# Optimization experiments

Hardware: AMD Instinct MI355X
Metric: run time of the kernel (lower is better)

Reference implementation:

```python
import jax, jax.numpy as jnp
from jax import lax
import numpy as np

B, N, F_IN = 8, 8192, 64
NPOINT, K = 2048, 16
C0 = F_IN + 3  # use_xyz concat
EPS = 1e-5


def setup_inputs() -> dict:
    key = jax.random.key(0)
    ks = jax.random.split(key, 8)
    xyz = jax.random.normal(ks[0], (B, 3, N), dtype=jnp.float32)
    points = jax.random.normal(ks[1], (B, F_IN, N), dtype=jnp.float32)
    def conv_params(k, cout, cin):
        W = jax.random.normal(k, (cout, cin), dtype=jnp.float32) * (1.0 / np.sqrt(cin))
        return W, jnp.zeros((cout,), jnp.float32)
    W1, b1 = conv_params(ks[2], 64, C0)
    W2, b2 = conv_params(ks[3], 64, 64)
    W3, b3 = conv_params(ks[4], 128, 64)
    g1 = jnp.ones((64,), jnp.float32); be1 = jnp.zeros((64,), jnp.float32)
    g2 = jnp.ones((64,), jnp.float32); be2 = jnp.zeros((64,), jnp.float32)
    return dict(xyz=xyz, points=points, W1=W1, b1=b1, g1=g1, be1=be1,
                W2=W2, b2=b2, g2=g2, be2=be2, W3=W3, b3=b3)


def _fps(xyz_bn3, npoint):
    # furthest point sampling; starts at index 0 (as PointNet++ CUDA op)
    b, n, _ = xyz_bn3.shape
    init_idx = jnp.zeros((b,), jnp.int32)
    dist0 = jnp.full((b, n), 1e10, xyz_bn3.dtype)

    def body(carry, _):
        dist, last = carry
        p = jnp.take_along_axis(xyz_bn3, last[:, None, None], axis=1)  # (b,1,3)
        d = jnp.sum((xyz_bn3 - p) ** 2, axis=-1)                       # (b,n)
        dist = jnp.minimum(dist, d)
        nxt = jnp.argmax(dist, axis=-1).astype(jnp.int32)
        return (dist, nxt), nxt

    (_, _), rest = lax.scan(body, (dist0, init_idx), None, length=npoint - 1)
    return jnp.concatenate([init_idx[None], rest], axis=0).T  # (b, npoint)


def _gather_feat(feat, idx):
    # feat: (B,C,N), idx: (B,...) -> (B,C,...)
    return jax.vmap(lambda f, i: f[:, i])(feat, idx)


def _conv_bn_relu(x, W, b, g, be):
    # 1x1 Conv2d + BatchNorm2d(training batch stats) + ReLU
    y = jnp.einsum('oi,bipk->bopk', W, x) + b[None, :, None, None]
    mean = y.mean(axis=(0, 2, 3))
    var = y.var(axis=(0, 2, 3))
    y = (y - mean[None, :, None, None]) * lax.rsqrt(var + EPS)[None, :, None, None]
    y = y * g[None, :, None, None] + be[None, :, None, None]
    return jax.nn.relu(y)


def reference(xyz, points, W1, b1, g1, be1, W2, b2, g2, be2, W3, b3):
    # --- sample_and_group_knn ---
    xyz_t = jnp.transpose(xyz, (0, 2, 1))             # (B,N,3)
    fps_idx = _fps(xyz_t, NPOINT)                      # (B,npoint)
    new_xyz = _gather_feat(xyz, fps_idx)               # (B,3,npoint)
    q = jnp.transpose(new_xyz, (0, 2, 1))              # (B,npoint,3)
    # squared distances (B,npoint,N)
    sq = (jnp.sum(q ** 2, -1)[:, :, None]
          + jnp.sum(xyz_t ** 2, -1)[:, None, :]
          - 2.0 * jnp.einsum('bqc,bnc->bqn', q, xyz_t))
    _, idx = lax.top_k(-sq, K)                         # (B,npoint,K) nearest
    grouped_xyz = _gather_feat(xyz, idx)               # (B,3,npoint,K)
    grouped_xyz = grouped_xyz - new_xyz[:, :, :, None]
    grouped_pts = _gather_feat(points, idx)            # (B,f,npoint,K)
    new_points = jnp.concatenate([grouped_xyz, grouped_pts], axis=1)  # (B,67,npoint,K)
    # --- shared MLP (1x1 convs) + max-pool over neighbors ---
    h = _conv_bn_relu(new_points, W1, b1, g1, be1)
    h = _conv_bn_relu(h, W2, b2, g2, be2)
    h = jnp.einsum('oi,bipk->bopk', W3, h) + b3[None, :, None, None]  # no bn/act
    new_feat = jnp.max(h, axis=3)                      # (B,128,npoint)
    return new_xyz, new_feat
```

## Files before the change

### kernel.cpp

```cpp
#include <hip/hip_runtime.h>
#pragma clang fp contract(off)

#define BB 8
#define NN 8192
#define NP 2048
#define KNbr 16
#define FIN 64
#define NPOS (BB*NP*KNbr)

typedef float f32x2 __attribute__((ext_vector_type(2)));
typedef unsigned long long u64;

__device__ __forceinline__ float sq3(float x, float y, float z) {
  return __fadd_rn(__fadd_rn(__fmul_rn(x,x), __fmul_rn(y,y)), __fmul_rn(z,z));
}

__device__ __forceinline__ int wave_imax(int x) {
  x = max(x, __builtin_amdgcn_update_dpp(0, x, 0x111, 0xf, 0xf, false));
  x = max(x, __builtin_amdgcn_update_dpp(0, x, 0x112, 0xf, 0xf, false));
  x = max(x, __builtin_amdgcn_update_dpp(0, x, 0x114, 0xf, 0xf, false));
  x = max(x, __builtin_amdgcn_update_dpp(0, x, 0x118, 0xf, 0xf, false));
  x = max(x, __builtin_amdgcn_update_dpp(0, x, 0x142, 0xa, 0xf, false));
  x = max(x, __builtin_amdgcn_update_dpp(0, x, 0x143, 0xc, 0xf, false));
  return __builtin_amdgcn_readlane(x, 63);
}
__device__ __forceinline__ unsigned wave_umin(unsigned x) {
  x = min(x, (unsigned)__builtin_amdgcn_update_dpp(-1, (int)x, 0x111, 0xf, 0xf, false));
  x = min(x, (unsigned)__builtin_amdgcn_update_dpp(-1, (int)x, 0x112, 0xf, 0xf, false));
  x = min(x, (unsigned)__builtin_amdgcn_update_dpp(-1, (int)x, 0x114, 0xf, 0xf, false));
  x = min(x, (unsigned)__builtin_amdgcn_update_dpp(-1, (int)x, 0x118, 0xf, 0xf, false));
  x = min(x, (unsigned)__builtin_amdgcn_update_dpp(-1, (int)x, 0x142, 0xa, 0xf, false));
  x = min(x, (unsigned)__builtin_amdgcn_update_dpp(-1, (int)x, 0x143, 0xc, 0xf, false));
  return (unsigned)__builtin_amdgcn_readlane((int)x, 63);
}

__global__ __launch_bounds__(256,1) void k_front(const float* __restrict__ xyz,
                                                 const float* __restrict__ pts,
                                                 const float* __restrict__ W1,
                                                 const float* __restrict__ b1,
                                                 float4* __restrict__ xyzw,
                                                 float4* __restrict__ qw,
                                                 float* __restrict__ pre,
                                                 float* __restrict__ stats,
                                                 float* __restrict__ newxyz) {
  __shared__ float tx[NN], ty[NN], tz[NN];
  __shared__ float4 res[NP];
  __shared__ u64 skey[2][4];
  int blk = blockIdx.x, tid = threadIdx.x;

  if (blk >= 8) {
    int g = (blk-8)*256 + tid;
    int b = g >> 13, n = g & (NN-1);
    const float* p = xyz + (size_t)b*3*NN;
    float x = p[n], y = p[NN+n], z = p[2*NN+n];
    xyzw[g] = make_float4(x, y, z, sq3(x,y,z));
    if (blk == 8) stats[tid] = 0.f;
    const float* P = pts + (size_t)b*FIN*NN + n;
    float pv[64];
    #pragma unroll
    for (int i=0;i<64;++i) pv[i] = P[(size_t)i*NN];
    float4* outp = (float4*)(pre + (size_t)g*64);
    for (int og=0; og<16; ++og) {
      float acc[4];
      #pragma unroll
      for (int oo=0;oo<4;++oo) {
        int o = og*4+oo;
        float s = b1[o];
        #pragma unroll
        for (int i=0;i<64;++i) s = fmaf(W1[o*67+3+i], pv[i], s);
        acc[oo] = s;
      }
      outp[og] = make_float4(acc[0],acc[1],acc[2],acc[3]);
    }
    return;
  }

  int b = blk;
  const float* pxyz = xyz + (size_t)b*3*NN;
  f32x2 px[16], py[16], pz[16], d2[16];
  #pragma unroll
  for (int j=0;j<16;++j) {
    int i = j*512 + 2*tid;
    float2 xv = *(const float2*)(pxyz + i);
    float2 yv = *(const float2*)(pxyz + NN + i);
    float2 zv = *(const float2*)(pxyz + 2*NN + i);
    tx[i] = xv.x; tx[i+1] = xv.y;
    ty[i] = yv.x; ty[i+1] = yv.y;
    tz[i] = zv.x; tz[i+1] = zv.y;
    px[j] = f32x2{xv.x, xv.y};
    py[j] = f32x2{yv.x, yv.y};
    pz[j] = f32x2{zv.x, zv.y};
    d2[j] = f32x2{1e10f, 1e10f};
  }
  float cx = pxyz[0], cy = pxyz[NN], cz = pxyz[2*NN];
  if (tid==0) res[0] = make_float4(cx, cy, cz, __int_as_float(0));
  int w = tid>>6;
  __syncthreads();
  for (int t=1;t<NP;++t) {
    f32x2 cx2 = {cx,cx}, cy2 = {cy,cy}, cz2 = {cz,cz};
    #pragma unroll
    for (int j=0;j<16;++j) {
      f32x2 dx = px[j]-cx2, dy = py[j]-cy2, dz = pz[j]-cz2;
      f32x2 dd = (dx*dx + dy*dy) + dz*dz;
#if __has_builtin(__builtin_elementwise_min)
      d2[j] = __builtin_elementwise_min(d2[j], dd);
#else
      d2[j].x = fminf(d2[j].x, dd.x);
      d2[j].y = fminf(d2[j].y, dd.y);
#endif
    }
    float tv[16]; int tk[16];
    #pragma unroll
    for (int j=0;j<16;++j) {
      bool r = d2[j].y > d2[j].x;
      tv[j] = r ? d2[j].y : d2[j].x;
      tk[j] = r ? 2*j+1 : 2*j;
    }
    #pragma unroll
    for (int j=0;j<8;++j) { bool r = tv[j+8] > tv[j]; if (r){tv[j]=tv[j+8]; tk[j]=tk[j+8];} }
    #pragma unroll
    for (int j=0;j<4;++j) { bool r = tv[j+4] > tv[j]; if (r){tv[j]=tv[j+4]; tk[j]=tk[j+4];} }
    #pragma unroll
    for (int j=0;j<2;++j) { bool r = tv[j+2] > tv[j]; if (r){tv[j]=tv[j+2]; tk[j]=tk[j+2];} }
    bool rr = tv[1] > tv[0];
    float lmax = rr ? tv[1] : tv[0];
    int   k    = rr ? tk[1] : tk[0];
    unsigned gidx = (unsigned)((k>>1)*512 + 2*tid + (k&1));
    int mb = wave_imax(__float_as_int(lmax));
    unsigned cand = (__float_as_int(lmax) == mb) ? gidx : 0xFFFFFFFFu;
    unsigned wwin = wave_umin(cand);
    int buf = t & 1;
    if ((tid & 63) == 0)
      skey[buf][w] = ((u64)(unsigned)mb << 32) | (u64)(0xFFFFFFFFu - wwin);
    __syncthreads();
    u64 mk = skey[buf][0];
    if (skey[buf][1] > mk) mk = skey[buf][1];
    if (skey[buf][2] > mk) mk = skey[buf][2];
    if (skey[buf][3] > mk) mk = skey[buf][3];
    unsigned widx = 0xFFFFFFFFu - (unsigned)(mk & 0xFFFFFFFFull);
    cx = tx[widx]; cy = ty[widx]; cz = tz[widx];
    if (tid == (t & 255))
      res[t] = make_float4(cx, cy, cz, __int_as_float((int)widx));
  }
  __syncthreads();
  float* outx = newxyz + (size_t)b*3*NP;
  #pragma unroll
  for (int s=0;s<8;++s) {
    int i = s*256 + tid;
    float4 r = res[i];
    qw[b*NP + i] = make_float4(r.x, r.y, r.z, sq3(r.x, r.y, r.z));
    outx[i] = r.x; outx[NP + i] = r.y; outx[2*NP + i] = r.z;
  }
}

__global__ __launch_bounds__(256) void k_knn(const float4* __restrict__ xyzw,
                                             const float4* __restrict__ qw,
                                             int* __restrict__ knnid) {
  int wave = threadIdx.x >> 6, lane = threadIdx.x & 63;
  int q = blockIdx.x*4 + wave;
  int b = q >> 11;
  float4 Q = qw[q];
  const float4* base = xyzw + (size_t)b*NN;
  float ld = 3.0e38f; int li = 0x7fffffff;
  float taud = 3.0e38f; int taui = 0x7fffffff;
  for (int c = 0; c < 128; ++c) {
    int idx = c*64 + lane;
    float4 P = base[idx];
    float dot = __fadd_rn(__fadd_rn(__fmul_rn(P.x,Q.x), __fmul_rn(P.y,Q.y)), __fmul_rn(P.z,Q.z));
    float dd  = __fsub_rn(__fadd_rn(Q.w, P.w), __fmul_rn(2.0f, dot));
    bool better = (dd < taud) || (dd == taud && idx < taui);
    u64 mask = __ballot(better);
    while (mask) {
      int src = __ffsll(mask) - 1;
      mask &= mask - 1;
      float bd = __shfl(dd, src, 64);
      int   bi = __shfl(idx, src, 64);
      bool before = (ld < bd) || (ld == bd && li < bi);
      float sd = __shfl_up(ld, 1, 64);
      int   si = __shfl_up(li, 1, 64);
      int   bp = __shfl_up((int)before, 1, 64);
      bool take_new = !before && (lane == 0 || bp);
      float nd = before ? ld : (take_new ? bd : sd);
      int   ni = before ? li : (take_new ? bi : si);
      if (lane < 16) { ld = nd; li = ni; }
      taud = __shfl(ld, 15, 64);
      taui = __shfl(li, 15, 64);
    }
  }
  if (lane < 16) knnid[q*16 + lane] = li;
}

__global__ __launch_bounds__(256) void k_y1(const float4* __restrict__ xyzw,
                                            const float4* __restrict__ qw,
                                            const int* __restrict__ knn,
                                            const float* __restrict__ pre,
                                            const float* __restrict__ W1,
                                            float* __restrict__ y) {
  int pos = blockIdx.x*256 + threadIdx.x;
  int bq = pos >> 4;
  int b  = pos >> 15;
  int n  = knn[pos];
  float4 Q = qw[bq];
  float4 P = xyzw[(b<<13) + n];
  float dx = __fsub_rn(P.x,Q.x), dy = __fsub_rn(P.y,Q.y), dz = __fsub_rn(P.z,Q.z);
  const float4* pr = (const float4*)(pre + ((size_t)(b<<13)+n)*64);
  float4* out = (float4*)(y + (size_t)pos*64);
  for (int og=0; og<16; ++og) {
    float4 acc = pr[og];
    float a[4] = {acc.x, acc.y, acc.z, acc.w};
    #pragma unroll
    for (int oo=0;oo<4;++oo) {
      int o = og*4+oo;
      a[oo] = fmaf(W1[o*67+0], dx, fmaf(W1[o*67+1], dy, fmaf(W1[o*67+2], dz, a[oo])));
    }
    out[og] = make_float4(a[0],a[1],a[2],a[3]);
  }
}

__global__ __launch_bounds__(256) void k_stats(const float* __restrict__ y,
                                               float* __restrict__ st) {
  __shared__ float s1[256], s2[256];
  int tid = threadIdx.x; int c = tid & 63, r = tid >> 6;
  size_t base = (size_t)blockIdx.x * 1024;
  float sum = 0.f, ss = 0.f;
  for (int i=0;i<256;++i) {
    float v = y[(base + (size_t)i*4 + r)*64 + c];
    sum += v; ss = fmaf(v, v, ss);
  }
  s1[tid]=sum; s2[tid]=ss;
  __syncthreads();
  if (tid < 64) {
    float t1 = s1[tid]+s1[tid+64]+s1[tid+128]+s1[tid+192];
    float t2 = s2[tid]+s2[tid+64]+s2[tid+128]+s2[tid+192];
    atomicAdd(&st[tid], t1);
    atomicAdd(&st[64+tid], t2);
  }
}

__global__ __launch_bounds__(256) void k_act(float* __restrict__ y,
                                             const float* __restrict__ st,
                                             const float* __restrict__ gam,
                                             const float* __restrict__ bet) {
  __shared__ __align__(16) float sS[64], sT[64];
  int tid = threadIdx.x;
  if (tid < 64) {
    float mean = st[tid] * (1.0f/NPOS);
    float var  = st[64+tid] * (1.0f/NPOS) - mean*mean;
    float istd = 1.0f / sqrtf(var + 1e-5f);
    float s = gam[tid]*istd;
    sS[tid] = s;
    sT[tid] = bet[tid] - mean*s;
  }
  __syncthreads();
  size_t g = (size_t)blockIdx.x*256 + tid;
  float4* Y = (float4*)y;
  #pragma unroll
  for (int r=0;r<4;++r) {
    size_t f4 = g + (size_t)r*1048576;
    int c0 = (int)((f4*4) & 63);
    float4 s4 = *(const float4*)(sS + c0);
    float4 t4 = *(const float4*)(sT + c0);
    float4 v = Y[f4];
    v.x = fmaxf(0.f, fmaf(v.x, s4.x, t4.x));
    v.y = fmaxf(0.f, fmaf(v.y, s4.y, t4.y));
    v.z = fmaxf(0.f, fmaf(v.z, s4.z, t4.z));
    v.w = fmaxf(0.f, fmaf(v.w, s4.w, t4.w));
    Y[f4] = v;
  }
}

__device__ __forceinline__ float dot64(const float4* x, const float* W, float init) {
  float a0 = init, a1 = 0.f, a2 = 0.f, a3 = 0.f;
  #pragma unroll
  for (int j=0;j<16;++j) {
    float4 v = x[j];
    a0 = fmaf(v.x, W[4*j],   a0);
    a1 = fmaf(v.y, W[4*j+1], a1);
    a2 = fmaf(v.z, W[4*j+2], a2);
    a3 = fmaf(v.w, W[4*j+3], a3);
  }
  return (a0+a1)+(a2+a3);
}

__global__ __launch_bounds__(256) void k_conv2v(float* __restrict__ y,
                                                const float* __restrict__ W2,
                                                const float* __restrict__ b2,
                                                float* __restrict__ st2) {
  __shared__ float r1[4][64], r2[4][64];
  int wave = threadIdx.x>>6;
  int wid = blockIdx.x*4 + wave;
  int lane = threadIdx.x & 63;
  float W[64];
  #pragma unroll
  for (int j=0;j<16;++j) {
    float4 t = *(const float4*)(W2 + (size_t)lane*64 + j*4);
    W[4*j]=t.x; W[4*j+1]=t.y; W[4*j+2]=t.z; W[4*j+3]=t.w;
  }
  float bb = b2[lane];
  size_t p0 = (size_t)wid*128;
  const float4* src = (const float4*)(y + p0*64);
  float4 xa[16], xb[16];
  float sum = 0.f, ss = 0.f;
  #pragma unroll
  for (int j=0;j<16;++j) xa[j] = src[j];
  for (int p=0;p<128;p+=2) {
    #pragma unroll
    for (int j=0;j<16;++j) xb[j] = src[(p+1)*16 + j];
    float acc = dot64(xa, W, bb);
    y[(p0+p)*64 + lane] = acc;
    sum += acc; ss = fmaf(acc, acc, ss);
    if (p+2 < 128) {
      #pragma unroll
      for (int j=0;j<16;++j) xa[j] = src[(p+2)*16 + j];
    }
    float acc2 = dot64(xb, W, bb);
    y[(p0+p+1)*64 + lane] = acc2;
    sum += acc2; ss = fmaf(acc2, acc2, ss);
  }
  r1[wave][lane] = sum; r2[wave][lane] = ss;
  __syncthreads();
  if (threadIdx.x < 64) {
    int l = threadIdx.x;
    float t1 = r1[0][l]+r1[1][l]+r1[2][l]+r1[3][l];
    float t2 = r2[0][l]+r2[1][l]+r2[2][l]+r2[3][l];
    atomicAdd(&st2[l], t1);
    atomicAdd(&st2[64+l], t2);
  }
}

__global__ __launch_bounds__(256) void k_c3v(const float* __restrict__ y,
                                             const float* __restrict__ W3,
                                             const float* __restrict__ b3,
                                             float* __restrict__ feat) {
  int wid = blockIdx.x*4 + (threadIdx.x>>6);
  int lane = threadIdx.x & 63;
  int h = wid & 1, chunk = wid >> 1;
  float W[64];
  #pragma unroll
  for (int j=0;j<16;++j) {
    float4 t = *(const float4*)(W3 + ((size_t)(h*64+lane))*64 + j*4);
    W[4*j]=t.x; W[4*j+1]=t.y; W[4*j+2]=t.z; W[4*j+3]=t.w;
  }
  float bb = b3[h*64+lane];
  const float4* src = (const float4*)(y + (size_t)chunk*16*16*64);
  float4 xa[16], xb[16];
  #pragma unroll
  for (int j=0;j<16;++j) xa[j] = src[j];
  int pos = 0;
  for (int q=0;q<16;++q) {
    float m = -3.0e38f;
    #pragma unroll 1
    for (int k=0;k<16;k+=2) {
      #pragma unroll
      for (int j=0;j<16;++j) xb[j] = src[(pos+1)*16 + j];
      m = fmaxf(m, dot64(xa, W, bb));
      if (pos+2 < 256) {
        #pragma unroll
        for (int j=0;j<16;++j) xa[j] = src[(pos+2)*16 + j];
      }
      m = fmaxf(m, dot64(xb, W, bb));
      pos += 2;
    }
    int gq = chunk*16 + q;
    int b = gq >> 11, qq = gq & (NP-1);
    feat[((size_t)(b*128 + h*64 + lane))*NP + qq] = m;
  }
}

extern "C" void kernel_launch(void* const* d_in, const int* in_sizes, int n_in,
                              void* d_out, int out_size, void* d_ws, size_t ws_size,
                              hipStream_t stream) {
  const float* xyz = (const float*)d_in[0];
  const float* pts = (const float*)d_in[1];
  const float* W1  = (const float*)d_in[2];
  const float* b1  = (const float*)d_in[3];
  const float* g1  = (const float*)d_in[4];
  const float* be1 = (const float*)d_in[5];
  const float* W2  = (const float*)d_in[6];
  const float* b2  = (const float*)d_in[7];
  const float* g2  = (const float*)d_in[8];
  const float* be2 = (const float*)d_in[9];
  const float* W3  = (const float*)d_in[10];
  const float* b3  = (const float*)d_in[11];
  float* out = (float*)d_out;
  float* ws  = (float*)d_ws;

  float4* xyzw  = (float4*)ws;
  float4* qw    = (float4*)(ws + 262144);
  int*    knnid = (int*)(ws + 344064);
  float*  pre   = ws + 1654784;
  float*  ybuf  = ws + 5849088;
  float*  stats = ws + 22626304;

  k_front <<<264, 256, 0, stream>>>(xyz, pts, W1, b1, xyzw, qw, pre, stats, out);
  k_knn   <<<4096, 256, 0, stream>>>(xyzw, qw, knnid);
  k_y1    <<<1024, 256, 0, stream>>>(xyzw, qw, knnid, pre, W1, ybuf);
  k_stats <<<256, 256, 0, stream>>>(ybuf, stats);
  k_act   <<<4096, 256, 0, stream>>>(ybuf, stats, g1, be1);
  k_conv2v<<<512, 256, 0, stream>>>(ybuf, W2, b2, stats + 128);
  k_act   <<<4096, 256, 0, stream>>>(ybuf, stats + 128, g2, be2);
  k_c3v   <<<512, 256, 0, stream>>>(ybuf, W3, b3, out + 49152);
}
```

Measured before the change: 2.621 ms.

## Overlap KNN grouping with FPS via persistent consumer blocks and progress flags

Merges the FPS front kernel, KNN search, first-layer grouping and BN statistics into one persistent launch. Eight blocks run FPS and publish query points plus a per-batch progress counter. The other 248 blocks first compute the pointwise W1 projection, then wait on a grid-wide flag barrier. They then poll the progress counters and run KNN, the xyz-offset conv and the stat accumulation for each query as soon as it is published. This hides the serial FPS latency behind the KNN work and removes several kernel launches and the knn-index and stats passes. The risks are that correctness depends on all blocks being co-resident, and that the progress and barrier flags are never reset between calls, so on repeated calls consumers may proceed on stale state.

Result: no change. 2.594 ms (-1.0%).

```diff
diff --git a/kernel.cpp b/kernel.cpp
--- a/kernel.cpp
+++ b/kernel.cpp
@@ -7,6 +7,8 @@
 #define KNbr 16
 #define FIN 64
 #define NPOS (BB*NP*KNbr)
+#define NCONS 248
+#define AG __HIP_MEMORY_SCOPE_AGENT
 
 typedef float f32x2 __attribute__((ext_vector_type(2)));
 typedef unsigned long long u64;
@@ -34,44 +36,123 @@
   return (unsigned)__builtin_amdgcn_readlane((int)x, 63);
 }
 
-__global__ __launch_bounds__(256,1) void k_front(const float* __restrict__ xyz,
-                                                 const float* __restrict__ pts,
-                                                 const float* __restrict__ W1,
-                                                 const float* __restrict__ b1,
-                                                 float4* __restrict__ xyzw,
-                                                 float4* __restrict__ qw,
-                                                 float* __restrict__ pre,
-                                                 float* __restrict__ stats,
-                                                 float* __restrict__ newxyz) {
+__device__ __forceinline__ void qstore4(float* p, float x, float y, float z, float w) {
+  __hip_atomic_store(p+0, x, __ATOMIC_RELAXED, AG);
+  __hip_atomic_store(p+1, y, __ATOMIC_RELAXED, AG);
+  __hip_atomic_store(p+2, z, __ATOMIC_RELAXED, AG);
+  __hip_atomic_store(p+3, w, __ATOMIC_RELAXED, AG);
+}
+
+__global__ __launch_bounds__(256,1) void k_front2(const float* __restrict__ xyz,
+                                                  const float* __restrict__ pts,
+                                                  const float* __restrict__ W1,
+                                                  const float* __restrict__ b1,
+                                                  float4* __restrict__ xyzw,
+                                                  float* __restrict__ qwf,
+                                                  float* __restrict__ pre,
+                                                  float* __restrict__ stats,
+                                                  int* __restrict__ prog,
+                                                  int* __restrict__ pflag,
+                                                  float* __restrict__ ybuf,
+                                                  float* __restrict__ newxyz) {
   __shared__ float tx[NN], ty[NN], tz[NN];
   __shared__ float4 res[NP];
   __shared__ u64 skey[2][4];
   int blk = blockIdx.x, tid = threadIdx.x;
+  int lane = tid & 63, wave = tid >> 6;
 
   if (blk >= 8) {
-    int g = (blk-8)*256 + tid;
-    int b = g >> 13, n = g & (NN-1);
-    const float* p = xyz + (size_t)b*3*NN;
-    float x = p[n], y = p[NN+n], z = p[2*NN+n];
-    xyzw[g] = make_float4(x, y, z, sq3(x,y,z));
+    for (int g = (blk-8)*256 + tid; g < BB*NN; g += NCONS*256) {
+      int b = g >> 13, n = g & (NN-1);
+      const float* p = xyz + (size_t)b*3*NN;
+      float x = p[n], y = p[NN+n], z = p[2*NN+n];
+      xyzw[g] = make_float4(x, y, z, sq3(x,y,z));
+      const float* P = pts + (size_t)b*FIN*NN + n;
+      float pv[64];
+      #pragma unroll
+      for (int i=0;i<64;++i) pv[i] = P[(size_t)i*NN];
+      float4* outp = (float4*)(pre + (size_t)g*64);
+      for (int og=0; og<16; ++og) {
+        float acc[4];
+        #pragma unroll
+        for (int oo=0;oo<4;++oo) {
+          int o = og*4+oo;
+          float s = b1[o];
+          #pragma unroll
+          for (int i=0;i<64;++i) s = fmaf(W1[o*67+3+i], pv[i], s);
+          acc[oo] = s;
+        }
+        outp[og] = make_float4(acc[0],acc[1],acc[2],acc[3]);
+      }
+    }
     if (blk == 8) stats[tid] = 0.f;
-    const float* P = pts + (size_t)b*FIN*NN + n;
-    float pv[64];
-    #pragma unroll
-    for (int i=0;i<64;++i) pv[i] = P[(size_t)i*NN];
-    float4* outp = (float4*)(pre + (size_t)g*64);
-    for (int og=0; og<16; ++og) {
-      float acc[4];
-      #pragma unroll
-      for (int oo=0;oo<4;++oo) {
-        int o = og*4+oo;
-        float s = b1[o];
-        #pragma unroll
-        for (int i=0;i<64;++i) s = fmaf(W1[o*67+3+i], pv[i], s);
-        acc[oo] = s;
+    __syncthreads();
+    if (tid == 0) {
+      __threadfence();
+      __hip_atomic_store(&pflag[blk-8], 1, __ATOMIC_RELEASE, AG);
+    }
+    bool ok = false;
+    while (!ok) {
+      int v = 1;
+      for (int i = lane; i < NCONS; i += 64)
+        v &= (__hip_atomic_load(&pflag[i], __ATOMIC_RELAXED, AG) == 1);
+      ok = (bool)__all(v);
+      if (!ok) __builtin_amdgcn_s_sleep(32);
+    }
+    __threadfence();
+
+    int slot = (blk-8)*4 + wave;
+    float W1a = W1[lane*67+0], W1b = W1[lane*67+1], W1c = W1[lane*67+2];
+    float sum = 0.f, ss = 0.f;
+    for (int qi = slot; qi < BB*NP; qi += NCONS*4) {
+      int t = qi >> 3, b = qi & 7;
+      while (__hip_atomic_load(&prog[b], __ATOMIC_RELAXED, AG) <= t)
+        __builtin_amdgcn_s_sleep(16);
+      const float* qp = qwf + ((size_t)(b*NP + t))*4;
+      float qx  = __hip_atomic_load(qp+0, __ATOMIC_RELAXED, AG);
+      float qy  = __hip_atomic_load(qp+1, __ATOMIC_RELAXED, AG);
+      float qz  = __hip_atomic_load(qp+2, __ATOMIC_RELAXED, AG);
+      float qw4 = __hip_atomic_load(qp+3, __ATOMIC_RELAXED, AG);
+      const float4* base = xyzw + (size_t)b*NN;
+      float ld = 3.0e38f; int li = 0x7fffffff;
+      float taud = 3.0e38f; int taui = 0x7fffffff;
+      for (int c = 0; c < 128; ++c) {
+        int idx = c*64 + lane;
+        float4 P = base[idx];
+        float dot = __fadd_rn(__fadd_rn(__fmul_rn(P.x,qx), __fmul_rn(P.y,qy)), __fmul_rn(P.z,qz));
+        float dd  = __fsub_rn(__fadd_rn(qw4, P.w), __fmul_rn(2.0f, dot));
+        bool better = (dd < taud) || (dd == taud && idx < taui);
+        u64 mask = __ballot(better);
+        while (mask) {
+          int src = __ffsll(mask) - 1;
+          mask &= mask - 1;
+          float bd = __shfl(dd, src, 64);
+          int   bi = __shfl(idx, src, 64);
+          bool before = (ld < bd) || (ld == bd && li < bi);
+          float sd = __shfl_up(ld, 1, 64);
+          int   si = __shfl_up(li, 1, 64);
+          int   bp = __shfl_up((int)before, 1, 64);
+          bool take_new = !before && (lane == 0 || bp);
+          float nd = before ? ld : (take_new ? bd : sd);
+          int   ni = before ? li : (take_new ? bi : si);
+          if (lane < 16) { ld = nd; li = ni; }
+          taud = __shfl(ld, 15, 64);
+          taui = __shfl(li, 15, 64);
+        }
       }
-      outp[og] = make_float4(acc[0],acc[1],acc[2],acc[3]);
-    }
+      const float* preb = pre + (size_t)b*NN*64;
+      float* yb = ybuf + ((size_t)(b*NP + t))*16*64;
+      for (int l=0;l<16;++l) {
+        int n = __shfl(li, l, 64);
+        float4 P = base[n];
+        float dx=__fsub_rn(P.x,qx), dy=__fsub_rn(P.y,qy), dz=__fsub_rn(P.z,qz);
+        float v = fmaf(W1a, dx, fmaf(W1b, dy, fmaf(W1c, dz, preb[(size_t)n*64 + lane])));
+        yb[l*64 + lane] = v;
+        sum += v; ss = fmaf(v, v, ss);
+      }
+    }
+    atomicAdd(&stats[lane], sum);
+    atomicAdd(&stats[64+lane], ss);
     return;
   }
 
@@ -93,7 +174,11 @@
     d2[j] = f32x2{1e10f, 1e10f};
   }
   float cx = pxyz[0], cy = pxyz[NN], cz = pxyz[2*NN];
-  if (tid==0) res[0] = make_float4(cx, cy, cz, __int_as_float(0));
+  if (tid==0) {
+    res[0] = make_float4(cx, cy, cz, 0.f);
+    qstore4(qwf + (size_t)(b*NP)*4, cx, cy, cz, sq3(cx,cy,cz));
+    __hip_atomic_store(&prog[b], 1, __ATOMIC_RELEASE, AG);
+  }
   int w = tid>>6;
   __syncthreads();
   for (int t=1;t<NP;++t) {
@@ -133,107 +218,27 @@
     if ((tid & 63) == 0)
       skey[buf][w] = ((u64)(unsigned)mb << 32) | (u64)(0xFFFFFFFFu - wwin);
     __syncthreads();
+    if ((t & 7) == 0 && tid == 0)
+      __hip_atomic_store(&prog[b], t, __ATOMIC_RELEASE, AG);
     u64 mk = skey[buf][0];
     if (skey[buf][1] > mk) mk = skey[buf][1];
     if (skey[buf][2] > mk) mk = skey[buf][2];
     if (skey[buf][3] > mk) mk = skey[buf][3];
     unsigned widx = 0xFFFFFFFFu - (unsigned)(mk & 0xFFFFFFFFull);
     cx = tx[widx]; cy = ty[widx]; cz = tz[widx];
-    if (tid == (t & 255))
-      res[t] = make_float4(cx, cy, cz, __int_as_float((int)widx));
+    if (tid == (t & 255)) {
+      res[t] = make_float4(cx, cy, cz, 0.f);
+      qstore4(qwf + ((size_t)(b*NP + t))*4, cx, cy, cz, sq3(cx,cy,cz));
+    }
   }
   __syncthreads();
+  if (tid == 0) __hip_atomic_store(&prog[b], NP, __ATOMIC_RELEASE, AG);
   float* outx = newxyz + (size_t)b*3*NP;
   #pragma unroll
   for (int s=0;s<8;++s) {
     int i = s*256 + tid;
     float4 r = res[i];
-    qw[b*NP + i] = make_float4(r.x, r.y, r.z, sq3(r.x, r.y, r.z));
     outx[i] = r.x; outx[NP + i] = r.y; outx[2*NP + i] = r.z;
-  }
-}
-
-__global__ __launch_bounds__(256) void k_knn(const float4* __restrict__ xyzw,
-                                             const float4* __restrict__ qw,
-                                             int* __restrict__ knnid) {
-  int wave = threadIdx.x >> 6, lane = threadIdx.x & 63;
-  int q = blockIdx.x*4 + wave;
-  int b = q >> 11;
-  float4 Q = qw[q];
-  const float4* base = xyzw + (size_t)b*NN;
-  float ld = 3.0e38f; int li = 0x7fffffff;
-  float taud = 3.0e38f; int taui = 0x7fffffff;
-  for (int c = 0; c < 128; ++c) {
-    int idx = c*64 + lane;
-    float4 P = base[idx];
-    float dot = __fadd_rn(__fadd_rn(__fmul_rn(P.x,Q.x), __fmul_rn(P.y,Q.y)), __fmul_rn(P.z,Q.z));
-    float dd  = __fsub_rn(__fadd_rn(Q.w, P.w), __fmul_rn(2.0f, dot));
-    bool better = (dd < taud) || (dd == taud && idx < taui);
-    u64 mask = __ballot(better);
-    while (mask) {
-      int src = __ffsll(mask) - 1;
-      mask &= mask - 1;
-      float bd = __shfl(dd, src, 64);
-      int   bi = __shfl(idx, src, 64);
-      bool before = (ld < bd) || (ld == bd && li < bi);
-      float sd = __shfl_up(ld, 1, 64);
-      int   si = __shfl_up(li, 1, 64);
-      int   bp = __shfl_up((int)before, 1, 64);
-      bool take_new = !before && (lane == 0 || bp);
-      float nd = before ? ld : (take_new ? bd : sd);
-      int   ni = before ? li : (take_new ? bi : si);
-      if (lane < 16) { ld = nd; li = ni; }
-      taud = __shfl(ld, 15, 64);
-      taui = __shfl(li, 15, 64);
-    }
-  }
-  if (lane < 16) knnid[q*16 + lane] = li;
-}
-
-__global__ __launch_bounds__(256) void k_y1(const float4* __restrict__ xyzw,
-                                            const float4* __restrict__ qw,
-                                            const int* __restrict__ knn,
-                                            const float* __restrict__ pre,
-                                            const float* __restrict__ W1,
-                                            float* __restrict__ y) {
-  int pos = blockIdx.x*256 + threadIdx.x;
-  int bq = pos >> 4;
-  int b  = pos >> 15;
-  int n  = knn[pos];
-  float4 Q = qw[bq];
-  float4 P = xyzw[(b<<13) + n];
-  float dx = __fsub_rn(P.x,Q.x), dy = __fsub_rn(P.y,Q.y), dz = __fsub_rn(P.z,Q.z);
-  const float4* pr = (const float4*)(pre + ((size_t)(b<<13)+n)*64);
-  float4* out = (float4*)(y + (size_t)pos*64);
-  for (int og=0; og<16; ++og) {
-    float4 acc = pr[og];
-    float a[4] = {acc.x, acc.y, acc.z, acc.w};
-    #pragma unroll
-    for (int oo=0;oo<4;++oo) {
-      int o = og*4+oo;
-      a[oo] = fmaf(W1[o*67+0], dx, fmaf(W1[o*67+1], dy, fmaf(W1[o*67+2], dz, a[oo])));
-    }
-    out[og] = make_float4(a[0],a[1],a[2],a[3]);
-  }
-}
-
-__global__ __launch_bounds__(256) void k_stats(const float* __restrict__ y,
-                                               float* __restrict__ st) {
-  __shared__ float s1[256], s2[256];
-  int tid = threadIdx.x; int c = tid & 63, r = tid >> 6;
-  size_t base = (size_t)blockIdx.x * 1024;
-  float sum = 0.f, ss = 0.f;
-  for (int i=0;i<256;++i) {
-    float v = y[(base + (size_t)i*4 + r)*64 + c];
-    sum += v; ss = fmaf(v, v, ss);
-  }
-  s1[tid]=sum; s2[tid]=ss;
-  __syncthreads();
-  if (tid < 64) {
-    float t1 = s1[tid]+s1[tid+64]+s1[tid+128]+s1[tid+192];
-    float t2 = s2[tid]+s2[tid+64]+s2[tid+128]+s2[tid+192];
-    atomicAdd(&st[tid], t1);
-    atomicAdd(&st[64+tid], t2);
   }
 }
 
@@ -386,16 +391,15 @@
   float* ws  = (float*)d_ws;
 
   float4* xyzw  = (float4*)ws;
-  float4* qw    = (float4*)(ws + 262144);
-  int*    knnid = (int*)(ws + 344064);
+  float*  qwf   = ws + 262144;
   float*  pre   = ws + 1654784;
   float*  ybuf  = ws + 5849088;
   float*  stats = ws + 22626304;
-
-  k_front <<<264, 256, 0, stream>>>(xyz, pts, W1, b1, xyzw, qw, pre, stats, out);
-  k_knn   <<<4096, 256, 0, stream>>>(xyzw, qw, knnid);
-  k_y1    <<<1024, 256, 0, stream>>>(xyzw, qw, knnid, pre, W1, ybuf);
-  k_stats <<<256, 256, 0, stream>>>(ybuf, stats);
+  int*    prog  = (int*)(ws + 22626560);
+  int*    pflag = (int*)(ws + 22626568);
+
+  k_front2<<<256, 256, 0, stream>>>(xyz, pts, W1, b1, xyzw, qwf, pre, stats,
+                                    prog, pflag, ybuf, out);
   k_act   <<<4096, 256, 0, stream>>>(ybuf, stats, g1, be1);
   k_conv2v<<<512, 256, 0, stream>>>(ybuf, W2, b2, stats + 128);
   k_act   <<<4096, 256, 0, stream>>>(ybuf, stats + 128, g2, be2);
```
